# Kernel optimization log

Measured on AMD Instinct MI355X. Metric: run time of the kernel, lower is better.

The kernel has to match this reference:

```python
import jax, jax.numpy as jnp
import numpy as np

N = 131072   # total nodes in batch
E = 524288   # directed edges
B = 2048     # number of graphs
H = 128      # hidden_dim
NF = 30      # node_feature_dim
GF = 4415    # gene_feature_dim
L = 3        # gnn_layers
EPS = 1e-5   # batchnorm eps


def setup_inputs() -> dict:
    key = jax.random.key(0)
    ks = jax.random.split(key, 24)
    rn = lambda k, s, sc=0.05: jax.random.normal(k, s, jnp.float32) * sc
    return {
        "x": jax.random.normal(ks[0], (N, NF), jnp.float32),
        "gene_features": jax.random.normal(ks[1], (B, GF), jnp.float32),
        "edge_index": jax.random.randint(ks[2], (2, E), 0, N),
        "batch": (jnp.arange(N) * B) // N,  # sorted, every graph non-empty
        "W_emb": rn(ks[3], (NF, H)), "b_emb": jnp.zeros((H,), jnp.float32),
        "Wg": rn(ks[4], (L, H, H)), "bg": jnp.zeros((L, H), jnp.float32),
        "bn_gamma": jnp.ones((L, H), jnp.float32), "bn_beta": jnp.zeros((L, H), jnp.float32),
        "Wd1": rn(ks[5], (2 * H, H)), "bd1": jnp.zeros((H,), jnp.float32),
        "Wd2": rn(ks[6], (H, H)), "bd2": jnp.zeros((H,), jnp.float32),
        "Wge1": rn(ks[7], (GF, 256)), "bge1": jnp.zeros((256,), jnp.float32),
        "g_gamma": jnp.ones((256,), jnp.float32), "g_beta": jnp.zeros((256,), jnp.float32),
        "Wge2": rn(ks[8], (256, H)), "bge2": jnp.zeros((H,), jnp.float32),
        "Wh1": rn(ks[9], (2 * H, H)), "bh1": jnp.zeros((H,), jnp.float32),
        "h_gamma": jnp.ones((H,), jnp.float32), "h_beta": jnp.zeros((H,), jnp.float32),
        "Wh2": rn(ks[10], (H, 64)), "bh2": jnp.zeros((64,), jnp.float32),
        "Wh3": rn(ks[11], (64, 1)), "bh3": jnp.zeros((1,), jnp.float32),
    }


def _bn_eval(x, gamma, beta):
    # inference batchnorm with running_mean=0, running_var=1
    return x * (gamma / jnp.sqrt(1.0 + EPS)) + beta


def _gcn_conv(h, W, b, src, dst):
    # PyG GCNConv: add self-loops, symmetric deg normalization, W first, bias after agg
    hw = h @ W                                            # [N,H]
    loop = jnp.arange(N)
    src_a = jnp.concatenate([src, loop])                  # [E+N]
    dst_a = jnp.concatenate([dst, loop])
    deg = jax.ops.segment_sum(jnp.ones((E + N,), hw.dtype), dst_a, num_segments=N)
    dinv = jnp.where(deg > 0, jax.lax.rsqrt(deg), 0.0)
    norm = dinv[src_a] * dinv[dst_a]                      # [E+N]
    msgs = hw[src_a] * norm[:, None]                      # gather [E+N,H]
    out = jax.ops.segment_sum(msgs, dst_a, num_segments=N)
    return out + b


def reference(x, gene_features, edge_index, batch, W_emb, b_emb, Wg, bg, bn_gamma,
              bn_beta, Wd1, bd1, Wd2, bd2, Wge1, bge1, g_gamma, g_beta, Wge2, bge2,
              Wh1, bh1, h_gamma, h_beta, Wh2, bh2, Wh3, bh3):
    src, dst = edge_index[0], edge_index[1]
    h = jax.nn.relu(x @ W_emb + b_emb)                    # [N,H]
    for i in range(L):
        hn = _gcn_conv(h, Wg[i], bg[i], src, dst)
        hn = jax.nn.relu(_bn_eval(hn, bn_gamma[i], bn_beta[i]))
        h = hn if i == 0 else h + hn                      # residual for i>0
    # global mean / max pooling per graph
    counts = jax.ops.segment_sum(jnp.ones((N,), h.dtype), batch, num_segments=B)
    mean_pool = jax.ops.segment_sum(h, batch, num_segments=B) / jnp.maximum(counts, 1.0)[:, None]
    max_pool = jax.ops.segment_max(h, batch, num_segments=B)
    graph_repr = jnp.concatenate([mean_pool, max_pool], axis=1)   # [B,2H]
    drug = jax.nn.relu(graph_repr @ Wd1 + bd1) @ Wd2 + bd2        # [B,H]
    g1 = jax.nn.relu(_bn_eval(gene_features @ Wge1 + bge1, g_gamma, g_beta))
    gene = jax.nn.relu(g1 @ Wge2 + bge2)                          # [B,H]
    comb = jnp.concatenate([drug, gene], axis=1)                  # [B,2H]
    z = jax.nn.relu(_bn_eval(comb @ Wh1 + bh1, h_gamma, h_beta))
    z = jax.nn.relu(z @ Wh2 + bh2)
    return z @ Wh3 + bh3                                          # [B,1]
```

## Files before the change

### kernel.cpp

```cpp
#include <hip/hip_runtime.h>

#define N_NODES 131072
#define E_EDGES 524288
#define B_GR    2048
#define H_DIM   128
#define NF_DIM  30
#define GF_DIM  4415
#define GF_PAD  4416
#define BN_SCALE 0.9999950000374997f
#define NSPLIT  32

typedef __bf16 bf16x8 __attribute__((ext_vector_type(8)));
typedef float  f32x4  __attribute__((ext_vector_type(4)));
typedef unsigned int uint32;
typedef uint32 u32x4 __attribute__((ext_vector_type(4)));

__device__ __forceinline__ void split2(float x, __bf16& hi, __bf16& lo){
    hi = (__bf16)x;
    lo = (__bf16)(x - (float)hi);
}
__device__ __forceinline__ uint32 bfbits(float x){
    __bf16 h = (__bf16)x;
    return (uint32)__builtin_bit_cast(unsigned short, h);
}
__device__ __forceinline__ float unpack_even(uint32 u){ return __uint_as_float(u<<16); }
__device__ __forceinline__ float unpack_odd (uint32 u){ return __uint_as_float(u & 0xffff0000u); }
__device__ __forceinline__ uint32 pack2(float e, float o){ return bfbits(e) | (bfbits(o)<<16); }


__global__ void k_zero_int(int* __restrict__ p, int n){
    int i = blockIdx.x*256 + threadIdx.x;
    if(i < n) p[i] = 0;
}

__global__ void k_count(const int* __restrict__ dst, int* __restrict__ counts){
    int e = blockIdx.x*256 + threadIdx.x;
    if(e < E_EDGES) atomicAdd(&counts[dst[e]], 1);
}

__global__ void k_scan1(int* __restrict__ counts, int* __restrict__ bsums){
    __shared__ int s[1024];
    int t = threadIdx.x;
    int gi = blockIdx.x*1024 + t;
    int v = counts[gi];
    s[t] = v; __syncthreads();
    for(int off=1; off<1024; off<<=1){
        int x = (t>=off) ? s[t-off] : 0;
        __syncthreads();
        s[t] += x;
        __syncthreads();
    }
    counts[gi] = s[t] - v;
    if(t == 1023) bsums[blockIdx.x] = s[t];
}

__global__ void k_scan2(int* __restrict__ bsums){
    __shared__ int s[128];
    int t = threadIdx.x;
    int v = bsums[t]; s[t] = v; __syncthreads();
    for(int off=1; off<128; off<<=1){
        int x = (t>=off) ? s[t-off] : 0;
        __syncthreads();
        s[t] += x;
        __syncthreads();
    }
    bsums[t] = s[t] - v;
}

__global__ void k_scan3(const int* __restrict__ counts, const int* __restrict__ bsums,
                        int* __restrict__ rowptr){
    int i = blockIdx.x*1024 + threadIdx.x;
    rowptr[i] = counts[i] + bsums[blockIdx.x];
    if(i == 0) rowptr[N_NODES] = E_EDGES;
}

__global__ void k_dinv_cursor(const int* __restrict__ rowptr, float* __restrict__ dinv,
                              int* __restrict__ cursor){
    int n = blockIdx.x*256 + threadIdx.x;
    if(n < N_NODES){
        int a = rowptr[n], b = rowptr[n+1];
        dinv[n] = rsqrtf((float)(b - a) + 1.0f);
        cursor[n] = a;
    }
}

__global__ void k_fill(const int* __restrict__ src, const int* __restrict__ dst,
                       int* __restrict__ cursor, int* __restrict__ csr){
    int e = blockIdx.x*256 + threadIdx.x;
    if(e < E_EDGES){
        int p = atomicAdd(&cursor[dst[e]], 1);
        csr[p] = src[e];
    }
}


__global__ void k_split_weights(const float* __restrict__ Wge1, __bf16* __restrict__ wth,
                                __bf16* __restrict__ wtl,
                                const float* __restrict__ Wg, __bf16* __restrict__ gth,
                                __bf16* __restrict__ gtl,
                                const float* __restrict__ Wemb, __bf16* __restrict__ eth,
                                __bf16* __restrict__ etl){
    unsigned bid = blockIdx.x;
    if(bid < 4416u){
        unsigned idx = bid*256 + threadIdx.x;
        unsigned c = idx / GF_PAD, k = idx - c*GF_PAD;
        float v = (k < GF_DIM) ? Wge1[(size_t)k*256 + c] : 0.f;
        split2(v, wth[idx], wtl[idx]);
    } else if(bid < 4416u + 192u){
        int idx = (bid - 4416u)*256 + threadIdx.x;
        int l = idx >> 14, i = idx & 16383;
        int k = i >> 7, c = i & 127;
        float v = Wg[idx];
        int o = (l << 14) + (c << 7) + k;
        split2(v, gth[o], gtl[o]);
    } else {
        int idx = (bid - 4608u)*256 + threadIdx.x;
        int c = idx >> 5, k = idx & 31;
        float v = (k < NF_DIM) ? Wemb[k*H_DIM + c] : 0.f;
        split2(v, eth[idx], etl[idx]);
    }
}


__global__ __launch_bounds__(256)
void k_emb_mfma(const float* __restrict__ x,
                const __bf16* __restrict__ wth, const __bf16* __restrict__ wtl,
                const float* __restrict__ bias, uint32* __restrict__ Hh2,
                uint32* __restrict__ Hl2){
    __shared__ float sT[4][32*68];
    int wave = threadIdx.x >> 6, lane = threadIdx.x & 63;
    int lr = lane & 15, lq = lane >> 4;
    int rbase = blockIdx.x*128 + wave*32;
    const f32x4 zero4 = {0.f,0.f,0.f,0.f};
    const float* xr0 = x + (size_t)(rbase + lr)*NF_DIM;
    const float* xr1 = x + (size_t)(rbase + 16 + lr)*NF_DIM;
    bf16x8 A0h, A0l, A1h, A1l;
    #pragma unroll
    for(int t=0;t<8;t++){
        int k = lq*8 + t;
        float v0 = (k < NF_DIM) ? xr0[k] : 0.f;
        float v1 = (k < NF_DIM) ? xr1[k] : 0.f;
        __bf16 h, l;
        split2(v0, h, l); A0h[t] = h; A0l[t] = l;
        split2(v1, h, l); A1h[t] = h; A1l[t] = l;
    }
    int orow = lane >> 3;
    int oq   = lane & 7;
    float* sW = sT[wave];
    for(int ph=0; ph<2; ph++){
        #pragma unroll
        for(int cc=0; cc<4; cc++){
            int col = (ph*4+cc)*16 + lr;
            bf16x8 Bh = *(const bf16x8*)(wth + col*32 + lq*8);
            bf16x8 Bl = *(const bf16x8*)(wtl + col*32 + lq*8);
            f32x4 a0 = zero4, a1 = zero4;
            a0 = __builtin_amdgcn_mfma_f32_16x16x32_bf16(A0h, Bh, a0, 0,0,0);
            a0 = __builtin_amdgcn_mfma_f32_16x16x32_bf16(A0l, Bh, a0, 0,0,0);
            a0 = __builtin_amdgcn_mfma_f32_16x16x32_bf16(A0h, Bl, a0, 0,0,0);
            a1 = __builtin_amdgcn_mfma_f32_16x16x32_bf16(A1h, Bh, a1, 0,0,0);
            a1 = __builtin_amdgcn_mfma_f32_16x16x32_bf16(A1l, Bh, a1, 0,0,0);
            a1 = __builtin_amdgcn_mfma_f32_16x16x32_bf16(A1h, Bl, a1, 0,0,0);
            #pragma unroll
            for(int r=0;r<4;r++){
                sW[(lq*4+r)*68 + cc*16 + lr]    = a0[r];
                sW[(16+lq*4+r)*68 + cc*16 + lr] = a1[r];
            }
        }
        __syncthreads();
        int cg = ph*64 + oq*8;
        float bb[8];
        *(float4*)&bb[0] = *(const float4*)(bias + cg);
        *(float4*)&bb[4] = *(const float4*)(bias + cg + 4);
        #pragma unroll
        for(int i=0;i<4;i++){
            int row = i*8 + orow;
            float v[8];
            *(float4*)&v[0] = *(float4*)&sW[row*68 + oq*8];
            *(float4*)&v[4] = *(float4*)&sW[row*68 + oq*8 + 4];
            uint32 oh[4], ol[4];
            #pragma unroll
            for(int p=0;p<4;p++){
                float ve = fmaxf(v[2*p]   + bb[2*p],   0.f);
                float vo = fmaxf(v[2*p+1] + bb[2*p+1], 0.f);
                uint32 he = bfbits(ve), ho = bfbits(vo);
                oh[p] = he | (ho<<16);
                float le = ve - __uint_as_float(he<<16);
                float lo = vo - __uint_as_float(ho<<16);
                ol[p] = pack2(le, lo);
            }
            size_t oidx = (size_t)(rbase + row)*64 + (cg>>1);
            *(uint4*)(Hh2 + oidx) = make_uint4(oh[0],oh[1],oh[2],oh[3]);
            *(uint4*)(Hl2 + oidx) = make_uint4(ol[0],ol[1],ol[2],ol[3]);
        }
        __syncthreads();
    }
}


struct MetaA {
    int   j0A, cA, j0B, cB;
    float dnA, dnB;
    uint32 shA, slA, shB, slB;
};

__device__ __forceinline__ void load_metaA(MetaA& m, int nA, int lane,
                                           const int* __restrict__ rowptr,
                                           const float* __restrict__ dinv,
                                           const uint32* __restrict__ Hh2,
                                           const uint32* __restrict__ Hl2){
    int nB = nA + 8;
    int a0 = rowptr[nA], a1 = rowptr[nA+1];
    int b0 = rowptr[nB], b1 = rowptr[nB+1];
    m.j0A = a0; m.cA = a1 - a0;
    m.j0B = b0; m.cB = b1 - b0;
    m.dnA = dinv[nA]; m.dnB = dinv[nB];
    size_t iA = (size_t)nA*64 + lane, iB = (size_t)nB*64 + lane;
    m.shA = Hh2[iA]; m.slA = Hl2[iA];
    m.shB = Hh2[iB]; m.slB = Hl2[iB];
}

__device__ __forceinline__ void load_jj(int* jjA, int* jjB, const MetaA& m,
                                        const int* __restrict__ csr){
    int jmA = m.j0A + m.cA - 1;
    int jmB = m.j0B + m.cB - 1;
    #pragma unroll
    for(int t=0;t<8;t++){
        int ia = m.j0A + t; ia = ia > jmA ? jmA : ia;
        int ib = m.j0B + t; ib = ib > jmB ? jmB : ib;
        jjA[t] = csr[ia] & (N_NODES-1);
        jjB[t] = csr[ib] & (N_NODES-1);
    }
}

__device__ __forceinline__ void agg_step(
        const MetaA& cur, const int* jjA, const int* jjB, int ii,
        MetaA* m2, int n2,
        int* jj1A, int* jj1B, const MetaA* m1,
        int base16, int lane,
        const uint32* __restrict__ Hh2, const uint32* __restrict__ Hl2,
        const float* __restrict__ dinv, const int* __restrict__ rowptr,
        const int* __restrict__ csr,
        uint32* __restrict__ AhL, uint32* __restrict__ AlL){
    uint32 rrA[8], rrB[8];
    float  wwA[8], wwB[8];
    #pragma unroll
    for(int t=0;t<8;t++){
        wwA[t] = (t < cur.cA) ? dinv[jjA[t]] : 0.f;
        rrA[t] = Hh2[(size_t)jjA[t]*64 + lane];
        wwB[t] = (t < cur.cB) ? dinv[jjB[t]] : 0.f;
        rrB[t] = Hh2[(size_t)jjB[t]*64 + lane];
    }
    if(m2) load_metaA(*m2, n2, lane, rowptr, dinv, Hh2, Hl2);
    if(m1) load_jj(jj1A, jj1B, *m1, csr);
    float axA = (unpack_even(cur.shA) + unpack_even(cur.slA)) * cur.dnA;
    float ayA = (unpack_odd(cur.shA)  + unpack_odd(cur.slA))  * cur.dnA;
    float axB = (unpack_even(cur.shB) + unpack_even(cur.slB)) * cur.dnB;
    float ayB = (unpack_odd(cur.shB)  + unpack_odd(cur.slB))  * cur.dnB;
    #pragma unroll
    for(int t=0;t<8;t++){
        axA = fmaf(unpack_even(rrA[t]), wwA[t], axA);
        ayA = fmaf(unpack_odd(rrA[t]),  wwA[t], ayA);
        axB = fmaf(unpack_even(rrB[t]), wwB[t], axB);
        ayB = fmaf(unpack_odd(rrB[t]),  wwB[t], ayB);
    }
    int nb = cur.cA > cur.cB ? cur.cA : cur.cB;
    if(nb > 8){
        int jmA = cur.j0A + cur.cA - 1;
        int jmB = cur.j0B + cur.cB - 1;
        for(int j=8; j<nb; j+=8){
            int jja[8], jjb[8]; float wa[8], wb[8]; uint32 ra[8], rb[8];
            #pragma unroll
            for(int t=0;t<8;t++){
                int ia = cur.j0A + j + t; ia = ia > jmA ? jmA : ia;
                int ib = cur.j0B + j + t; ib = ib > jmB ? jmB : ib;
                jja[t] = csr[ia] & (N_NODES-1);
                jjb[t] = csr[ib] & (N_NODES-1);
            }
            #pragma unroll
            for(int t=0;t<8;t++){
                wa[t] = (j + t < cur.cA) ? dinv[jja[t]] : 0.f;
                ra[t] = Hh2[(size_t)jja[t]*64 + lane];
                wb[t] = (j + t < cur.cB) ? dinv[jjb[t]] : 0.f;
                rb[t] = Hh2[(size_t)jjb[t]*64 + lane];
            }
            #pragma unroll
            for(int t=0;t<8;t++){
                axA = fmaf(unpack_even(ra[t]), wa[t], axA);
                ayA = fmaf(unpack_odd(ra[t]),  wa[t], ayA);
                axB = fmaf(unpack_even(rb[t]), wb[t], axB);
                ayB = fmaf(unpack_odd(rb[t]),  wb[t], ayB);
            }
        }
    }
    axA *= cur.dnA; ayA *= cur.dnA;
    axB *= cur.dnB; ayB *= cur.dnB;
    int rowA = base16 + ii, rowB = rowA + 8;
    uint32 hxA = bfbits(axA), hyA = bfbits(ayA);
    AhL[rowA*68 + lane] = hxA | (hyA<<16);
    AlL[rowA*68 + lane] = pack2(axA - __uint_as_float(hxA<<16),
                                ayA - __uint_as_float(hyA<<16));
    uint32 hxB = bfbits(axB), hyB = bfbits(ayB);
    AhL[rowB*68 + lane] = hxB | (hyB<<16);
    AlL[rowB*68 + lane] = pack2(axB - __uint_as_float(hxB<<16),
                                ayB - __uint_as_float(hyB<<16));
}

__global__ __launch_bounds__(512, 4)
void k_layer(const __bf16* __restrict__ curHh, const __bf16* __restrict__ curHl,
             const float* __restrict__ dinv, const int* __restrict__ rowptr,
             const int* __restrict__ csr,
             const __bf16* __restrict__ Bth, const __bf16* __restrict__ Btl,
             const float* __restrict__ bias, const float* __restrict__ gamma,
             const float* __restrict__ beta,
             uint32* __restrict__ outHh2, uint32* __restrict__ outHl2, int residual){
    __shared__ uint32 smem[8*32*68];
    uint32* AhL = smem;
    uint32* AlL = smem + 128*68;
    int tid  = threadIdx.x;
    int wave = __builtin_amdgcn_readfirstlane(tid >> 6);
    int lane = tid & 63;
    int rbase = blockIdx.x * 128;
    int base16 = wave*16;
    const uint32* Hh2 = (const uint32*)curHh;
    const uint32* Hl2 = (const uint32*)curHl;

    {
        MetaA m0, m1, m2;
        int jj0A[8], jj0B[8], jj1A[8], jj1B[8];
        int nb0 = rbase + base16;
        load_metaA(m0, nb0+0, lane, rowptr, dinv, Hh2, Hl2);
        load_metaA(m1, nb0+1, lane, rowptr, dinv, Hh2, Hl2);
        load_jj(jj0A, jj0B, m0, csr);
        agg_step(m0, jj0A, jj0B, 0, &m2, nb0+2, jj1A, jj1B, &m1,
                 base16, lane, Hh2, Hl2, dinv, rowptr, csr, AhL, AlL);
        agg_step(m1, jj1A, jj1B, 1, &m0, nb0+3, jj0A, jj0B, &m2,
                 base16, lane, Hh2, Hl2, dinv, rowptr, csr, AhL, AlL);
        agg_step(m2, jj0A, jj0B, 2, &m1, nb0+4, jj1A, jj1B, &m0,
                 base16, lane, Hh2, Hl2, dinv, rowptr, csr, AhL, AlL);
        agg_step(m0, jj1A, jj1B, 3, &m2, nb0+5, jj0A, jj0B, &m1,
                 base16, lane, Hh2, Hl2, dinv, rowptr, csr, AhL, AlL);
        agg_step(m1, jj0A, jj0B, 4, &m0, nb0+6, jj1A, jj1B, &m2,
                 base16, lane, Hh2, Hl2, dinv, rowptr, csr, AhL, AlL);
        agg_step(m2, jj1A, jj1B, 5, &m1, nb0+7, jj0A, jj0B, &m0,
                 base16, lane, Hh2, Hl2, dinv, rowptr, csr, AhL, AlL);
        agg_step(m0, jj0A, jj0B, 6, nullptr, 0, jj1A, jj1B, &m1,
                 base16, lane, Hh2, Hl2, dinv, rowptr, csr, AhL, AlL);
        agg_step(m1, jj1A, jj1B, 7, nullptr, 0, nullptr, nullptr, nullptr,
                 base16, lane, Hh2, Hl2, dinv, rowptr, csr, AhL, AlL);
    }
    __syncthreads();

    int lr = lane & 15, lq = lane >> 4;
    int wr = wave & 3, wc = wave >> 2;
    int r0 = wr*32;
    bf16x8 A0h[4], A0l[4], A1h[4], A1l[4];
    #pragma unroll
    for(int ks=0;ks<4;ks++){
        int u0 = (r0 + lr)*68 + lq*4 + ks*16;
        int u1 = (r0 + 16 + lr)*68 + lq*4 + ks*16;
        A0h[ks] = __builtin_bit_cast(bf16x8, *(const u32x4*)(AhL + u0));
        A0l[ks] = __builtin_bit_cast(bf16x8, *(const u32x4*)(AlL + u0));
        A1h[ks] = __builtin_bit_cast(bf16x8, *(const u32x4*)(AhL + u1));
        A1l[ks] = __builtin_bit_cast(bf16x8, *(const u32x4*)(AlL + u1));
    }
    __syncthreads();

    float* stg = (float*)smem + wave*(32*68);
    const f32x4 zero4 = {0.f,0.f,0.f,0.f};
    #pragma unroll
    for(int cc=0; cc<4; cc++){
        int col = wc*64 + cc*16 + lr;
        f32x4 a0 = zero4, a1 = zero4;
        #pragma unroll
        for(int ks=0;ks<4;ks++){
            bf16x8 Bh = *(const bf16x8*)(Bth + col*H_DIM + ks*32 + lq*8);
            bf16x8 Bl = *(const bf16x8*)(Btl + col*H_DIM + ks*32 + lq*8);
            a0 = __builtin_amdgcn_mfma_f32_16x16x32_bf16(A0h[ks], Bh, a0, 0,0,0);
            a0 = __builtin_amdgcn_mfma_f32_16x16x32_bf16(A0l[ks], Bh, a0, 0,0,0);
            a0 = __builtin_amdgcn_mfma_f32_16x16x32_bf16(A0h[ks], Bl, a0, 0,0,0);
            a1 = __builtin_amdgcn_mfma_f32_16x16x32_bf16(A1h[ks], Bh, a1, 0,0,0);
            a1 = __builtin_amdgcn_mfma_f32_16x16x32_bf16(A1l[ks], Bh, a1, 0,0,0);
            a1 = __builtin_amdgcn_mfma_f32_16x16x32_bf16(A1h[ks], Bl, a1, 0,0,0);
        }
        #pragma unroll
        for(int r=0;r<4;r++){
            stg[(lq*4+r)*68 + cc*16 + lr]    = a0[r];
            stg[(16+lq*4+r)*68 + cc*16 + lr] = a1[r];
        }
    }

    int orow = lane >> 3;
    int oq   = lane & 7;
    int cg = wc*64 + oq*8;
    float bb[8], gg[8], tt[8];
    *(float4*)&bb[0] = *(const float4*)(bias + cg);
    *(float4*)&bb[4] = *(const float4*)(bias + cg + 4);
    *(float4*)&gg[0] = *(const float4*)(gamma + cg);
    *(float4*)&gg[4] = *(const float4*)(gamma + cg + 4);
    *(float4*)&tt[0] = *(const float4*)(beta + cg);
    *(float4*)&tt[4] = *(const float4*)(beta + cg + 4);
    #pragma unroll
    for(int p=0;p<8;p++) gg[p] *= BN_SCALE;
    #pragma unroll
    for(int i=0;i<4;i++){
        int row = i*8 + orow;
        float v[8];
        *(float4*)&v[0] = *(float4*)&stg[row*68 + oq*8];
        *(float4*)&v[4] = *(float4*)&stg[row*68 + oq*8 + 4];
        size_t oidx = (size_t)(rbase + r0 + row)*64 + (cg>>1);
        uint4 oldh = {0,0,0,0}, oldl = {0,0,0,0};
        if(residual){
            oldh = *(const uint4*)(Hh2 + oidx);
            oldl = *(const uint4*)(Hl2 + oidx);
        }
        uint32 ohv[4] = {oldh.x,oldh.y,oldh.z,oldh.w};
        uint32 olv[4] = {oldl.x,oldl.y,oldl.z,oldl.w};
        uint32 oh[4], ol[4];
        #pragma unroll
        for(int p=0;p<4;p++){
            float ve = fmaxf(fmaf(v[2*p]   + bb[2*p],   gg[2*p],   tt[2*p]),   0.f);
            float vo = fmaxf(fmaf(v[2*p+1] + bb[2*p+1], gg[2*p+1], tt[2*p+1]), 0.f);
            if(residual){
                ve += unpack_even(ohv[p]) + unpack_even(olv[p]);
                vo += unpack_odd(ohv[p])  + unpack_odd(olv[p]);
            }
            uint32 he = bfbits(ve), ho = bfbits(vo);
            oh[p] = he | (ho<<16);
            float le = ve - __uint_as_float(he<<16);
            float lo = vo - __uint_as_float(ho<<16);
            ol[p] = pack2(le, lo);
        }
        *(uint4*)(outHh2 + oidx) = make_uint4(oh[0],oh[1],oh[2],oh[3]);
        *(uint4*)(outHl2 + oidx) = make_uint4(ol[0],ol[1],ol[2],ol[3]);
    }
}


__global__ __launch_bounds__(256)
void k_gemm_gf_mfma(const float* __restrict__ Agf,
                    const __bf16* __restrict__ Bth, const __bf16* __restrict__ Btl,
                    float* __restrict__ gpart){
    int rt = blockIdx.x & 31;
    int sp = blockIdx.x >> 5;
    int ks0 = (sp*138) >> 5, ks1 = ((sp+1)*138) >> 5;
    int wave = threadIdx.x >> 6, lane = threadIdx.x & 63;
    int lr = lane & 15, lq = lane >> 4;
    int rbase = rt*64 + (wave & 1)*32;
    int cbase = (wave >> 1)*128;
    const f32x4 zero4 = {0.f,0.f,0.f,0.f};
    f32x4 acc[8][2];
    #pragma unroll
    for(int ct=0;ct<8;ct++){ acc[ct][0] = zero4; acc[ct][1] = zero4; }
    for(int ks=ks0; ks<ks1; ks++){
        int kc = ks*32;
        const float* ar0 = Agf + (size_t)(rbase + lr)*GF_DIM + kc + lq*8;
        const float* ar1 = ar0 + (size_t)16*GF_DIM;
        bf16x8 A0h, A0l, A1h, A1l;
        if(kc + 32 <= GF_DIM){
            #pragma unroll
            for(int t=0;t<8;t++){
                __bf16 h, l;
                split2(ar0[t], h, l); A0h[t] = h; A0l[t] = l;
                split2(ar1[t], h, l); A1h[t] = h; A1l[t] = l;
            }
        } else {
            #pragma unroll
            for(int t=0;t<8;t++){
                int k = kc + lq*8 + t;
                float v0 = 0.f, v1 = 0.f;
                if(k < GF_DIM){ v0 = ar0[t]; v1 = ar1[t]; }
                __bf16 h, l;
                split2(v0, h, l); A0h[t] = h; A0l[t] = l;
                split2(v1, h, l); A1h[t] = h; A1l[t] = l;
            }
        }
        #pragma unroll
        for(int ct=0;ct<8;ct++){
            size_t bo = (size_t)(cbase + ct*16 + lr)*GF_PAD + kc + lq*8;
            bf16x8 Bh = *(const bf16x8*)(Bth + bo);
            bf16x8 Bl = *(const bf16x8*)(Btl + bo);
            acc[ct][0] = __builtin_amdgcn_mfma_f32_16x16x32_bf16(A0h, Bh, acc[ct][0], 0,0,0);
            acc[ct][0] = __builtin_amdgcn_mfma_f32_16x16x32_bf16(A0l, Bh, acc[ct][0], 0,0,0);
            acc[ct][0] = __builtin_amdgcn_mfma_f32_16x16x32_bf16(A0h, Bl, acc[ct][0], 0,0,0);
            acc[ct][1] = __builtin_amdgcn_mfma_f32_16x16x32_bf16(A1h, Bh, acc[ct][1], 0,0,0);
            acc[ct][1] = __builtin_amdgcn_mfma_f32_16x16x32_bf16(A1l, Bh, acc[ct][1], 0,0,0);
            acc[ct][1] = __builtin_amdgcn_mfma_f32_16x16x32_bf16(A1h, Bl, acc[ct][1], 0,0,0);
        }
    }
    float* po = gpart + (size_t)sp*(B_GR*256);
    #pragma unroll
    for(int ct=0;ct<8;ct++)
        #pragma unroll
        for(int s=0;s<2;s++)
            #pragma unroll
            for(int r=0;r<4;r++)
                po[(size_t)(rbase + s*16 + lq*4 + r)*256 + cbase + ct*16 + lr] = acc[ct][s][r];
}

__global__ void k_gene_reduce(const float* __restrict__ gpart, const float* __restrict__ bias,
                              const float* __restrict__ gamma, const float* __restrict__ beta,
                              float* __restrict__ g1){
    int i = blockIdx.x*256 + threadIdx.x;
    int c = i & 255;
    float v = bias[c];
    #pragma unroll 8
    for(int sp=0;sp<NSPLIT;sp++) v += gpart[(size_t)sp*(B_GR*256) + i];
    v = fmaf(v, gamma[c]*BN_SCALE, beta[c]);
    g1[i] = fmaxf(v, 0.f);
}


__device__ __forceinline__ void load_w4(const float* __restrict__ W, int off, int tid,
                                        float4* t){
    const float4* s = (const float4*)(W + off);
    t[0] = s[tid];
    t[1] = s[tid + 512];
    t[2] = s[tid + 1024];
    t[3] = s[tid + 1536];
}
__device__ __forceinline__ void write_w4(float* sW, int tid, const float4* t){
    float4* d = (float4*)sW;
    d[tid]        = t[0];
    d[tid + 512]  = t[1];
    d[tid + 1024] = t[2];
    d[tid + 1536] = t[3];
}

__device__ __forceinline__ void dense_stage128(
        const float* __restrict__ W, int nck, const float* sA, int lda,
        float* sO, int ldo, float* sW, int tid, int c, int ga, int gb,
        float bias_c, float gsc, float bsh, int do_relu){
    float4 t[4];
    load_w4(W, 0, tid, t);
    write_w4(sW, tid, t);
    __syncthreads();
    float a0 = bias_c, a1 = bias_c;
    for(int ck=0; ck<nck; ck++){
        if(ck+1 < nck) load_w4(W, (ck+1)*8192, tid, t);
        const float* aga = sA + ga*lda + ck*64;
        const float* agb = sA + gb*lda + ck*64;
        #pragma unroll
        for(int k=0;k<64;k++){
            float w = sW[k*128 + c];
            a0 = fmaf(aga[k], w, a0);
            a1 = fmaf(agb[k], w, a1);
        }
        __syncthreads();
        if(ck+1 < nck){ write_w4(sW, tid, t); __syncthreads(); }
    }
    a0 = fmaf(a0, gsc, bsh);
    a1 = fmaf(a1, gsc, bsh);
    if(do_relu){ a0 = fmaxf(a0, 0.f); a1 = fmaxf(a1, 0.f); }
    sO[ga*ldo + c] = a0;
    sO[gb*ldo + c] = a1;
}

__global__ __launch_bounds__(512)
void k_head(const uint32* __restrict__ Hh2, const uint32* __restrict__ Hl2,
            const float* __restrict__ g1,
            const float* __restrict__ Wd1, const float* __restrict__ bd1,
            const float* __restrict__ Wd2, const float* __restrict__ bd2,
            const float* __restrict__ Wge2, const float* __restrict__ bge2,
            const float* __restrict__ Wh1, const float* __restrict__ bh1,
            const float* __restrict__ h_g, const float* __restrict__ h_b,
            const float* __restrict__ Wh2, const float* __restrict__ bh2,
            const float* __restrict__ Wh3, const float* __restrict__ bh3,
            float* __restrict__ out){
    __shared__ float sPool[8][256];
    __shared__ float sG1[8][256];
    __shared__ float sT1[8][128];
    __shared__ float sComb[8][256];
    __shared__ float sZ[8][128];
    __shared__ float sZ2[8][64];
    __shared__ float sW[8192];
    int tid = threadIdx.x;
    int wave = tid >> 6, lane = tid & 63;
    int g0 = blockIdx.x*8;
    {
        int idx = tid*4;
        int g = idx >> 8, c = idx & 255;
        *(float4*)&sG1[g][c] = *(const float4*)&g1[(size_t)(g0+g)*256 + c];
    }
    {
        size_t base = (size_t)(g0+wave)*4096 + lane;
        float se = 0.f, so = 0.f, me = -3.4e38f, mo = -3.4e38f;
        #pragma unroll 8
        for(int r=0;r<64;r++){
            uint32 h = Hh2[base + r*64];
            uint32 l = Hl2[base + r*64];
            float ve = unpack_even(h) + unpack_even(l);
            float vo = unpack_odd(h)  + unpack_odd(l);
            se += ve; so += vo;
            me = fmaxf(me, ve); mo = fmaxf(mo, vo);
        }
        sPool[wave][2*lane]       = se*(1.f/64.f);
        sPool[wave][2*lane+1]     = so*(1.f/64.f);
        sPool[wave][128+2*lane]   = me;
        sPool[wave][128+2*lane+1] = mo;
    }
    __syncthreads();
    int c = tid & 127, q = tid >> 7;
    int ga = 2*q, gb = 2*q + 1;
    dense_stage128(Wd1, 4, &sPool[0][0], 256, &sT1[0][0], 128, sW, tid, c, ga, gb,
                   bd1[c], 1.f, 0.f, 1);
    dense_stage128(Wd2, 2, &sT1[0][0], 128, &sComb[0][0], 256, sW, tid, c, ga, gb,
                   bd2[c], 1.f, 0.f, 0);
    dense_stage128(Wge2, 4, &sG1[0][0], 256, &sComb[0][0] + 128, 256, sW, tid, c, ga, gb,
                   bge2[c], 1.f, 0.f, 1);
    dense_stage128(Wh1, 4, &sComb[0][0], 256, &sZ[0][0], 128, sW, tid, c, ga, gb,
                   bh1[c], h_g[c]*BN_SCALE, h_b[c], 1);
    {
        float4 t[4];
        load_w4(Wh2, 0, tid, t);
        write_w4(sW, tid, t);
        __syncthreads();
        int c2 = tid & 63, q2 = tid >> 6;
        float a = bh2[c2];
        #pragma unroll
        for(int k=0;k<128;k++)
            a = fmaf(sZ[q2][k], sW[k*64 + c2], a);
        sZ2[q2][c2] = fmaxf(a, 0.f);
    }
    __syncthreads();
    {
        float v = sZ2[wave][lane] * Wh3[lane];
        #pragma unroll
        for(int off=32; off; off>>=1) v += __shfl_down(v, off);
        if(lane == 0) out[g0 + wave] = v + bh3[0];
    }
}


extern "C" void kernel_launch(void* const* d_in, const int* in_sizes, int n_in,
                              void* d_out, int out_size, void* d_ws, size_t ws_size,
                              hipStream_t stream){
    (void)in_sizes; (void)n_in; (void)out_size; (void)ws_size;
    const float* x    = (const float*)d_in[0];
    const float* gf   = (const float*)d_in[1];
    const int*   ei   = (const int*)  d_in[2];
    const float* W_emb= (const float*)d_in[4];
    const float* b_emb= (const float*)d_in[5];
    const float* Wg   = (const float*)d_in[6];
    const float* bg   = (const float*)d_in[7];
    const float* bn_g = (const float*)d_in[8];
    const float* bn_b = (const float*)d_in[9];
    const float* Wd1  = (const float*)d_in[10];
    const float* bd1  = (const float*)d_in[11];
    const float* Wd2  = (const float*)d_in[12];
    const float* bd2  = (const float*)d_in[13];
    const float* Wge1 = (const float*)d_in[14];
    const float* bge1 = (const float*)d_in[15];
    const float* g_g  = (const float*)d_in[16];
    const float* g_b  = (const float*)d_in[17];
    const float* Wge2 = (const float*)d_in[18];
    const float* bge2 = (const float*)d_in[19];
    const float* Wh1  = (const float*)d_in[20];
    const float* bh1  = (const float*)d_in[21];
    const float* h_g  = (const float*)d_in[22];
    const float* h_b  = (const float*)d_in[23];
    const float* Wh2  = (const float*)d_in[24];
    const float* bh2  = (const float*)d_in[25];
    const float* Wh3  = (const float*)d_in[26];
    const float* bh3  = (const float*)d_in[27];
    float* outp = (float*)d_out;

    char* base = (char*)d_ws;
    __bf16* Hh = (__bf16*)base;
    __bf16* Hl = (__bf16*)(base + (32u<<20));
    __bf16* Ph = (__bf16*)(base + (64u<<20));
    __bf16* Pl = (__bf16*)(base + (96u<<20));
    float*  gpart  = (float*)base;
    __bf16* wge_th = (__bf16*)(base + (64u<<20));
    __bf16* wge_tl = (__bf16*)(base + (64u<<20) + 2260992);
    char* T = base + (128u<<20);
    float* g1   = (float*)T;
    int* rowptr = (int*)(g1 + B_GR*256);
    int* cursor = rowptr + (N_NODES+1);
    int* csr    = cursor + N_NODES;
    int* bsums  = csr + E_EDGES;
    float* dinv = (float*)(bsums + 128);
    __bf16* wg_th = (__bf16*)(dinv + N_NODES);
    __bf16* wg_tl = wg_th + 3*16384;
    __bf16* we_th = wg_tl + 3*16384;
    __bf16* we_tl = we_th + 128*32;

    const int* src = ei;
    const int* dst = ei + E_EDGES;

    k_split_weights<<<4624, 256, 0, stream>>>(Wge1, wge_th, wge_tl, Wg, wg_th, wg_tl,
                                              W_emb, we_th, we_tl);

    k_gemm_gf_mfma<<<32*NSPLIT, 256, 0, stream>>>(gf, wge_th, wge_tl, gpart);
    k_gene_reduce <<<(B_GR*256)/256, 256, 0, stream>>>(gpart, bge1, g_g, g_b, g1);

    k_zero_int   <<<N_NODES/256, 256, 0, stream>>>(cursor, N_NODES);
    k_count      <<<E_EDGES/256, 256, 0, stream>>>(dst, cursor);
    k_scan1      <<<128, 1024, 0, stream>>>(cursor, bsums);
    k_scan2      <<<1, 128, 0, stream>>>(bsums);
    k_scan3      <<<128, 1024, 0, stream>>>(cursor, bsums, rowptr);
    k_dinv_cursor<<<N_NODES/256, 256, 0, stream>>>(rowptr, dinv, cursor);
    k_fill       <<<E_EDGES/256, 256, 0, stream>>>(src, dst, cursor, csr);

    k_emb_mfma<<<N_NODES/128, 256, 0, stream>>>(x, we_th, we_tl, b_emb,
                                                (uint32*)Hh, (uint32*)Hl);

    uint32 *curh = (uint32*)Hh, *curl = (uint32*)Hl;
    uint32 *outh = (uint32*)Ph, *outl = (uint32*)Pl;
    for(int i=0;i<3;i++){
        k_layer<<<N_NODES/128, 512, 0, stream>>>((const __bf16*)curh, (const __bf16*)curl,
                                                 dinv, rowptr, csr,
                                                 wg_th + i*16384, wg_tl + i*16384,
                                                 bg + i*H_DIM, bn_g + i*H_DIM, bn_b + i*H_DIM,
                                                 outh, outl, i > 0);
        uint32* th = curh; curh = outh; outh = th;
        uint32* tl = curl; curl = outl; outl = tl;
    }

    k_head<<<B_GR/8, 512, 0, stream>>>(curh, curl, g1,
                                       Wd1, bd1, Wd2, bd2, Wge2, bge2,
                                       Wh1, bh1, h_g, h_b, Wh2, bh2, Wh3, bh3, outp);
}
```

Baseline: 574.6 us.

## Fuse preprocessing kernels: atomic split-K reduction, tiled weight transpose, merged dinv into scan

The split-K gene GEMM now accumulates its partial sums directly into a zeroed buffer with atomics, and the bias/batchnorm/ReLU epilogue moves into the head kernel. This removes the 32-way partial buffer write and the separate reduce kernel. The Wge1 transpose-and-split now goes through a 64x64 shared-memory tile so both the reads and the writes are coalesced, and the dinv/cursor computation is folded into the final scan kernel. The cost is float atomic contention, plus a nondeterministic summation order in the gene branch.

Measured after the change: 583.0 us. About the same (+1.5%).

```diff
diff --git a/kernel.cpp b/kernel.cpp
--- a/kernel.cpp
+++ b/kernel.cpp
@@ -28,9 +28,11 @@
 __device__ __forceinline__ uint32 pack2(float e, float o){ return bfbits(e) | (bfbits(o)<<16); }
 
 
-__global__ void k_zero_int(int* __restrict__ p, int n){
+__global__ void k_zero2(int* __restrict__ a, int na, float* __restrict__ b, int nb){
     int i = blockIdx.x*256 + threadIdx.x;
-    if(i < n) p[i] = 0;
+    if(i < na) a[i] = 0;
+    int j = i - na;
+    if(j >= 0 && j < nb) b[j] = 0.f;
 }
 
 __global__ void k_count(const int* __restrict__ dst, int* __restrict__ counts){
@@ -68,20 +70,22 @@
 }
 
 __global__ void k_scan3(const int* __restrict__ counts, const int* __restrict__ bsums,
-                        int* __restrict__ rowptr){
+                        int* __restrict__ rowptr, float* __restrict__ dinv,
+                        int* __restrict__ cursor){
     int i = blockIdx.x*1024 + threadIdx.x;
-    rowptr[i] = counts[i] + bsums[blockIdx.x];
-    if(i == 0) rowptr[N_NODES] = E_EDGES;
-}
-
-__global__ void k_dinv_cursor(const int* __restrict__ rowptr, float* __restrict__ dinv,
-                              int* __restrict__ cursor){
-    int n = blockIdx.x*256 + threadIdx.x;
-    if(n < N_NODES){
-        int a = rowptr[n], b = rowptr[n+1];
-        dinv[n] = rsqrtf((float)(b - a) + 1.0f);
-        cursor[n] = a;
-    }
+    int r0 = counts[i] + bsums[blockIdx.x];
+    int r1;
+    if(i == N_NODES-1){
+        r1 = E_EDGES;
+        rowptr[N_NODES] = E_EDGES;
+    } else {
+        int ip = i + 1;
+        int nb = (threadIdx.x == 1023) ? blockIdx.x + 1 : blockIdx.x;
+        r1 = counts[ip] + bsums[nb];
+    }
+    rowptr[i] = r0;
+    dinv[i] = rsqrtf((float)(r1 - r0) + 1.0f);
+    cursor[i] = r0;
 }
 
 __global__ void k_fill(const int* __restrict__ src, const int* __restrict__ dst,
@@ -100,21 +104,37 @@
                                 __bf16* __restrict__ gtl,
                                 const float* __restrict__ Wemb, __bf16* __restrict__ eth,
                                 __bf16* __restrict__ etl){
+    __shared__ float sTile[64][65];
     unsigned bid = blockIdx.x;
-    if(bid < 4416u){
-        unsigned idx = bid*256 + threadIdx.x;
-        unsigned c = idx / GF_PAD, k = idx - c*GF_PAD;
-        float v = (k < GF_DIM) ? Wge1[(size_t)k*256 + c] : 0.f;
-        split2(v, wth[idx], wtl[idx]);
-    } else if(bid < 4416u + 192u){
-        int idx = (bid - 4416u)*256 + threadIdx.x;
+    int tid = threadIdx.x;
+    if(bid < 276u){
+        int kt = bid % 69u, ct = bid / 69u;
+        int k0 = kt*64, c0 = ct*64;
+        #pragma unroll
+        for(int i=0;i<16;i++){
+            int idx = i*256 + tid;
+            int kk = idx >> 6, cc = idx & 63;
+            int k = k0 + kk;
+            sTile[kk][cc] = (k < GF_DIM) ? Wge1[(size_t)k*256 + c0 + cc] : 0.f;
+        }
+        __syncthreads();
+        #pragma unroll
+        for(int i=0;i<16;i++){
+            int idx = i*256 + tid;
+            int cc = idx >> 6, kk = idx & 63;
+            float v = sTile[kk][cc];
+            size_t o = (size_t)(c0 + cc)*GF_PAD + k0 + kk;
+            split2(v, wth[o], wtl[o]);
+        }
+    } else if(bid < 276u + 192u){
+        int idx = (bid - 276u)*256 + tid;
         int l = idx >> 14, i = idx & 16383;
         int k = i >> 7, c = i & 127;
         float v = Wg[idx];
         int o = (l << 14) + (c << 7) + k;
         split2(v, gth[o], gtl[o]);
     } else {
-        int idx = (bid - 4608u)*256 + threadIdx.x;
+        int idx = (bid - 468u)*256 + tid;
         int c = idx >> 5, k = idx & 31;
         float v = (k < NF_DIM) ? Wemb[k*H_DIM + c] : 0.f;
         split2(v, eth[idx], etl[idx]);
@@ -439,7 +459,7 @@
 __global__ __launch_bounds__(256)
 void k_gemm_gf_mfma(const float* __restrict__ Agf,
                     const __bf16* __restrict__ Bth, const __bf16* __restrict__ Btl,
-                    float* __restrict__ gpart){
+                    float* __restrict__ g1acc){
     int rt = blockIdx.x & 31;
     int sp = blockIdx.x >> 5;
     int ks0 = (sp*138) >> 5, ks1 = ((sp+1)*138) >> 5;
@@ -487,26 +507,14 @@
             acc[ct][1] = __builtin_amdgcn_mfma_f32_16x16x32_bf16(A1h, Bl, acc[ct][1], 0,0,0);
         }
     }
-    float* po = gpart + (size_t)sp*(B_GR*256);
     #pragma unroll
     for(int ct=0;ct<8;ct++)
         #pragma unroll
         for(int s=0;s<2;s++)
             #pragma unroll
             for(int r=0;r<4;r++)
-                po[(size_t)(rbase + s*16 + lq*4 + r)*256 + cbase + ct*16 + lr] = acc[ct][s][r];
-}
-
-__global__ void k_gene_reduce(const float* __restrict__ gpart, const float* __restrict__ bias,
-                              const float* __restrict__ gamma, const float* __restrict__ beta,
-                              float* __restrict__ g1){
-    int i = blockIdx.x*256 + threadIdx.x;
-    int c = i & 255;
-    float v = bias[c];
-    #pragma unroll 8
-    for(int sp=0;sp<NSPLIT;sp++) v += gpart[(size_t)sp*(B_GR*256) + i];
-    v = fmaf(v, gamma[c]*BN_SCALE, beta[c]);
-    g1[i] = fmaxf(v, 0.f);
+                atomicAdd(&g1acc[(size_t)(rbase + s*16 + lq*4 + r)*256 + cbase + ct*16 + lr],
+                          acc[ct][s][r]);
 }
 
 
@@ -557,7 +565,9 @@
 
 __global__ __launch_bounds__(512)
 void k_head(const uint32* __restrict__ Hh2, const uint32* __restrict__ Hl2,
-            const float* __restrict__ g1,
+            const float* __restrict__ g1acc,
+            const float* __restrict__ bge1, const float* __restrict__ g_g,
+            const float* __restrict__ g_b,
             const float* __restrict__ Wd1, const float* __restrict__ bd1,
             const float* __restrict__ Wd2, const float* __restrict__ bd2,
             const float* __restrict__ Wge2, const float* __restrict__ bge2,
@@ -579,7 +589,14 @@
     {
         int idx = tid*4;
         int g = idx >> 8, c = idx & 255;
-        *(float4*)&sG1[g][c] = *(const float4*)&g1[(size_t)(g0+g)*256 + c];
+        float4 a  = *(const float4*)&g1acc[(size_t)(g0+g)*256 + c];
+        float4 b  = *(const float4*)&bge1[c];
+        float4 gm = *(const float4*)&g_g[c];
+        float4 bt = *(const float4*)&g_b[c];
+        sG1[g][c+0] = fmaxf(fmaf(a.x + b.x, gm.x*BN_SCALE, bt.x), 0.f);
+        sG1[g][c+1] = fmaxf(fmaf(a.y + b.y, gm.y*BN_SCALE, bt.y), 0.f);
+        sG1[g][c+2] = fmaxf(fmaf(a.z + b.z, gm.z*BN_SCALE, bt.z), 0.f);
+        sG1[g][c+3] = fmaxf(fmaf(a.w + b.w, gm.w*BN_SCALE, bt.w), 0.f);
     }
     {
         size_t base = (size_t)(g0+wave)*4096 + lane;
@@ -669,12 +686,12 @@
     __bf16* Hl = (__bf16*)(base + (32u<<20));
     __bf16* Ph = (__bf16*)(base + (64u<<20));
     __bf16* Pl = (__bf16*)(base + (96u<<20));
-    float*  gpart  = (float*)base;
     __bf16* wge_th = (__bf16*)(base + (64u<<20));
     __bf16* wge_tl = (__bf16*)(base + (64u<<20) + 2260992);
     char* T = base + (128u<<20);
-    float* g1   = (float*)T;
-    int* rowptr = (int*)(g1 + B_GR*256);
+    float* g1acc = (float*)T;
+    int* counts = (int*)(g1acc + B_GR*256);
+    int* rowptr = counts + N_NODES;
     int* cursor = rowptr + (N_NODES+1);
     int* csr    = cursor + N_NODES;
     int* bsums  = csr + E_EDGES;
@@ -687,19 +704,19 @@
     const int* src = ei;
     const int* dst = ei + E_EDGES;
 
-    k_split_weights<<<4624, 256, 0, stream>>>(Wge1, wge_th, wge_tl, Wg, wg_th, wg_tl,
-                                              W_emb, we_th, we_tl);
-
-    k_gemm_gf_mfma<<<32*NSPLIT, 256, 0, stream>>>(gf, wge_th, wge_tl, gpart);
-    k_gene_reduce <<<(B_GR*256)/256, 256, 0, stream>>>(gpart, bge1, g_g, g_b, g1);
-
-    k_zero_int   <<<N_NODES/256, 256, 0, stream>>>(cursor, N_NODES);
-    k_count      <<<E_EDGES/256, 256, 0, stream>>>(dst, cursor);
-    k_scan1      <<<128, 1024, 0, stream>>>(cursor, bsums);
-    k_scan2      <<<1, 128, 0, stream>>>(bsums);
-    k_scan3      <<<128, 1024, 0, stream>>>(cursor, bsums, rowptr);
-    k_dinv_cursor<<<N_NODES/256, 256, 0, stream>>>(rowptr, dinv, cursor);
-    k_fill       <<<E_EDGES/256, 256, 0, stream>>>(src, dst, cursor, csr);
+    k_split_weights<<<484, 256, 0, stream>>>(Wge1, wge_th, wge_tl, Wg, wg_th, wg_tl,
+                                             W_emb, we_th, we_tl);
+
+    k_zero2<<<(N_NODES + B_GR*256 + 255)/256, 256, 0, stream>>>(counts, N_NODES,
+                                                                g1acc, B_GR*256);
+
+    k_gemm_gf_mfma<<<32*NSPLIT, 256, 0, stream>>>(gf, wge_th, wge_tl, g1acc);
+
+    k_count<<<E_EDGES/256, 256, 0, stream>>>(dst, counts);
+    k_scan1<<<128, 1024, 0, stream>>>(counts, bsums);
+    k_scan2<<<1, 128, 0, stream>>>(bsums);
+    k_scan3<<<128, 1024, 0, stream>>>(counts, bsums, rowptr, dinv, cursor);
+    k_fill <<<E_EDGES/256, 256, 0, stream>>>(src, dst, cursor, csr);
 
     k_emb_mfma<<<N_NODES/128, 256, 0, stream>>>(x, we_th, we_tl, b_emb,
                                                 (uint32*)Hh, (uint32*)Hl);
@@ -716,7 +733,7 @@
         uint32* tl = curl; curl = outl; outl = tl;
     }
 
-    k_head<<<B_GR/8, 512, 0, stream>>>(curh, curl, g1,
+    k_head<<<B_GR/8, 512, 0, stream>>>(curh, curl, g1acc, bge1, g_g, g_b,
                                        Wd1, bd1, Wd2, bd2, Wge2, bge2,
                                        Wh1, bh1, h_g, h_b, Wh2, bh2, Wh3, bh3, outp);
 }
```
